# Optimization experiments

Hardware: AMD Instinct MI355X
Metric: run time of the kernel (lower is better)

Reference implementation:

```python
import jax, jax.numpy as jnp
import numpy as np

KEY_CHANNELS = 256


def conv1x1_relu(x, w, b):
    # x: [B, Cin, H, W], w: [Cout, Cin], b: [Cout] -> [B, Cout, H, W]
    y = jnp.einsum('oc,bchw->bohw', w, x) + b[None, :, None, None]
    return jax.nn.relu(y)


def setup_inputs() -> dict:
    key = jax.random.key(0)
    ks = jax.random.split(key, 16)
    B, C, H, W = 8, 512, 128, 128
    Kc, Kp = KEY_CHANNELS, 150
    sc = lambda cin: 1.0 / np.sqrt(cin)
    return {
        'x': jax.random.normal(ks[0], (B, C, H, W), jnp.float32),
        'proxy': jax.random.normal(ks[1], (B, C, Kp, 1), jnp.float32),
        'w_fp1': jax.random.normal(ks[2], (Kc, C), jnp.float32) * sc(C),
        'b_fp1': jax.random.normal(ks[3], (Kc,), jnp.float32) * 0.1,
        'w_fp2': jax.random.normal(ks[4], (Kc, Kc), jnp.float32) * sc(Kc),
        'b_fp2': jax.random.normal(ks[5], (Kc,), jnp.float32) * 0.1,
        'w_fo1': jax.random.normal(ks[6], (Kc, C), jnp.float32) * sc(C),
        'b_fo1': jax.random.normal(ks[7], (Kc,), jnp.float32) * 0.1,
        'w_fo2': jax.random.normal(ks[8], (Kc, Kc), jnp.float32) * sc(Kc),
        'b_fo2': jax.random.normal(ks[9], (Kc,), jnp.float32) * 0.1,
        'w_fd': jax.random.normal(ks[10], (Kc, C), jnp.float32) * sc(C),
        'b_fd': jax.random.normal(ks[11], (Kc,), jnp.float32) * 0.1,
        'w_fu': jax.random.normal(ks[12], (C, Kc), jnp.float32) * sc(Kc),
        'b_fu': jax.random.normal(ks[13], (C,), jnp.float32) * 0.1,
    }


def reference(x, proxy, w_fp1, b_fp1, w_fp2, b_fp2, w_fo1, b_fo1,
              w_fo2, b_fo2, w_fd, b_fd, w_fu, b_fu):
    B, C, H, W = x.shape
    Kc = w_fp1.shape[0]
    # f_pixel: two 1x1 conv(+folded BN)+ReLU blocks -> query [B, HW, Kc]
    q = conv1x1_relu(conv1x1_relu(x, w_fp1, b_fp1), w_fp2, b_fp2)
    query = q.reshape(B, Kc, H * W).transpose(0, 2, 1)
    # f_object -> key [B, Kc, Kp]
    k = conv1x1_relu(conv1x1_relu(proxy, w_fo1, b_fo1), w_fo2, b_fo2)
    key = k.reshape(B, Kc, -1)
    # f_down -> value [B, Kp, Kc]
    v = conv1x1_relu(proxy, w_fd, b_fd)
    value = v.reshape(B, Kc, -1).transpose(0, 2, 1)
    # cross-attention: softmax(Q K^T / sqrt(Kc)) V
    sim = jnp.einsum('bnc,bck->bnk', query, key) * (Kc ** -0.5)
    sim = jax.nn.softmax(sim, axis=-1)
    context = jnp.einsum('bnk,bkc->bnc', sim, value)  # [B, HW, Kc]
    context = context.transpose(0, 2, 1).reshape(B, Kc, H, W)
    # f_up: 1x1 conv(+folded BN)+ReLU back to in_channels
    return conv1x1_relu(context, w_fu, b_fu)
```

## Files before the change

### kernel.cpp

```cpp
#include <hip/hip_runtime.h>
#include <hip/hip_bf16.h>


typedef __bf16 bf16x8 __attribute__((ext_vector_type(8)));
typedef float f32x4 __attribute__((ext_vector_type(4)));
typedef unsigned short u16x8 __attribute__((ext_vector_type(8)));

#define AS1 __attribute__((address_space(1)))
#define AS3 __attribute__((address_space(3)))
#define MFMA_16x16x32(a, b, c) __builtin_amdgcn_mfma_f32_16x16x32_bf16((a), (b), (c), 0, 0, 0)

__device__ __forceinline__ unsigned short f2bf(float f) {
  union { float f; unsigned u; } x; x.f = f;
  unsigned r = (x.u + 0x7FFFu + ((x.u >> 16) & 1u)) >> 16;
  return (unsigned short)r;
}

__global__ __launch_bounds__(256) void cast_weights(
    const float* __restrict__ w1, const float* __restrict__ w2,
    const float* __restrict__ wu, unsigned short* __restrict__ W1b,
    unsigned short* __restrict__ W2b, unsigned short* __restrict__ Wub) {
  int i = blockIdx.x * 256 + threadIdx.x;
  if (i < 131072) W1b[i] = f2bf(w1[i]);
  else if (i < 196608) W2b[i - 131072] = f2bf(w2[i - 131072]);
  else if (i < 327680) Wub[i - 196608] = f2bf(wu[i - 196608]);
}

__global__ __launch_bounds__(256) void kv_kernel(
    const float* __restrict__ proxy,
    const float* __restrict__ w_fo1, const float* __restrict__ b_fo1,
    const float* __restrict__ w_fo2, const float* __restrict__ b_fo2,
    const float* __restrict__ w_fd, const float* __restrict__ b_fd,
    unsigned short* __restrict__ keyT, unsigned short* __restrict__ Vv) {
  __shared__ float cols[512][8];
  __shared__ float k1s[256][8];
  const int b = blockIdx.y;
  const int p0 = blockIdx.x * 8;
  const int t = threadIdx.x;
#pragma unroll
  for (int i = 0; i < 8; i++) {
    int idx = t + i * 256;
    int c = idx >> 2, q = idx & 3;
    int p = p0 + q * 2;
    float2 v = make_float2(0.f, 0.f);
    if (p < 150) v = *(const float2*)(proxy + ((size_t)b * 512 + c) * 150 + p);
    cols[c][q * 2 + 0] = v.x;
    cols[c][q * 2 + 1] = v.y;
  }
  __syncthreads();
  float accV[8], accK[8];
  {
    float bv = b_fd[t], bk = b_fo1[t];
#pragma unroll
    for (int px = 0; px < 8; px++) { accV[px] = bv; accK[px] = bk; }
  }
#define KV_FMA(j, wv_, wk_)                                      \
  { float4 ca = *(const float4*)&cols[c + j][0];                 \
    float4 cb = *(const float4*)&cols[c + j][4];                 \
    accV[0] += wv_ * ca.x; accV[1] += wv_ * ca.y;                \
    accV[2] += wv_ * ca.z; accV[3] += wv_ * ca.w;                \
    accV[4] += wv_ * cb.x; accV[5] += wv_ * cb.y;                \
    accV[6] += wv_ * cb.z; accV[7] += wv_ * cb.w;                \
    accK[0] += wk_ * ca.x; accK[1] += wk_ * ca.y;                \
    accK[2] += wk_ * ca.z; accK[3] += wk_ * ca.w;                \
    accK[4] += wk_ * cb.x; accK[5] += wk_ * cb.y;                \
    accK[6] += wk_ * cb.z; accK[7] += wk_ * cb.w; }
  for (int c = 0; c < 512; c += 4) {
    float4 wv4 = *(const float4*)(w_fd + (size_t)t * 512 + c);
    float4 wk4 = *(const float4*)(w_fo1 + (size_t)t * 512 + c);
    KV_FMA(0, wv4.x, wk4.x)
    KV_FMA(1, wv4.y, wk4.y)
    KV_FMA(2, wv4.z, wk4.z)
    KV_FMA(3, wv4.w, wk4.w)
  }
#pragma unroll
  for (int px = 0; px < 8; px++) {
    Vv[((size_t)b * 256 + t) * 160 + p0 + px] = f2bf(fmaxf(accV[px], 0.f));
    k1s[t][px] = fmaxf(accK[px], 0.f);
  }
  __syncthreads();
  float accY[8];
  {
    float by = b_fo2[t];
#pragma unroll
    for (int px = 0; px < 8; px++) accY[px] = by;
  }
#define KV_FMA2(j, wy_)                                          \
  { float4 ca = *(const float4*)&k1s[c + j][0];                  \
    float4 cb = *(const float4*)&k1s[c + j][4];                  \
    accY[0] += wy_ * ca.x; accY[1] += wy_ * ca.y;                \
    accY[2] += wy_ * ca.z; accY[3] += wy_ * ca.w;                \
    accY[4] += wy_ * cb.x; accY[5] += wy_ * cb.y;                \
    accY[6] += wy_ * cb.z; accY[7] += wy_ * cb.w; }
  for (int c = 0; c < 256; c += 4) {
    float4 wy4 = *(const float4*)(w_fo2 + (size_t)t * 256 + c);
    KV_FMA2(0, wy4.x)
    KV_FMA2(1, wy4.y)
    KV_FMA2(2, wy4.z)
    KV_FMA2(3, wy4.w)
  }
#pragma unroll
  for (int px = 0; px < 8; px++)
    keyT[((size_t)b * 160 + p0 + px) * 256 + t] = f2bf(fmaxf(accY[px], 0.f));
}

__global__ __launch_bounds__(256, 3) void gemm1_fused(
    const float* __restrict__ X, const unsigned short* __restrict__ Bt,
    const float* __restrict__ bias, unsigned short* __restrict__ Cq) {
  const int HW = 16384, K = 512, N = 256;
  __shared__ float Af[64 * 128];
  __shared__ unsigned short Bs[128 * 64];
  const int r = blockIdx.x;
  const int b = blockIdx.y;
  const int my = ((r >> 4) << 3) | (r & 7);
  const int nx = (r >> 3) & 1;
  const int m0 = my * 128, n0 = nx * 128;
  const int tid = threadIdx.x;
  const int w = tid >> 6, l = tid & 63;
  const int lr = l & 15, lg = l >> 4;
  const int wm = (w >> 1) * 64, wn = (w & 1) * 64;
  const float* Xb = X + (size_t)b * K * HW;
  const unsigned short* Btb = Bt + (size_t)n0 * K;
  const f32x4 zero = {0.f, 0.f, 0.f, 0.f};
  f32x4 acc[4][4];
#pragma unroll
  for (int m = 0; m < 4; m++)
#pragma unroll
    for (int n = 0; n < 4; n++) acc[m][n] = zero;

  const int arow = l >> 5;
  const int acol = l & 31;
  const int bsub = l >> 3;
  const int bcol = (l & 7) * 8;
  for (int kt = 0; kt < K; kt += 64) {
    __syncthreads();
#pragma unroll
    for (int i = 0; i < 8; i++) {
      const int rk = w * 16 + i * 2 + arow;
      const int s = (rk >> 3) & 7;
      __builtin_amdgcn_global_load_lds(
          (AS1 void*)(Xb + (size_t)(kt + rk) * HW + m0 + ((acol ^ s) << 2)),
          (AS3 void*)(Af + (w * 16 + i * 2) * 128), 16, 0, 0);
    }
#pragma unroll
    for (int i = 0; i < 4; i++) {
      __builtin_amdgcn_global_load_lds(
          (AS1 void*)(Btb + (size_t)(w * 32 + i * 8 + bsub) * K + kt + bcol),
          (AS3 void*)(Bs + (w * 32 + i * 8) * 64), 16, 0, 0);
    }
    __syncthreads();
#pragma unroll
    for (int ks = 0; ks < 2; ks++) {
      bf16x8 aF[4], bF[4];
      const int s = ks * 4 + lg;
#pragma unroll
      for (int m = 0; m < 4; m++) {
        const int p = wm + m * 16 + lr;
        const int cb = ((((p >> 2) ^ s) << 2) | (p & 3));
        bf16x8 a;
#pragma unroll
        for (int j = 0; j < 8; j++)
          a[j] = (__bf16)Af[(ks * 32 + lg * 8 + j) * 128 + cb];
        aF[m] = a;
      }
#pragma unroll
      for (int n = 0; n < 4; n++)
        bF[n] = *(const bf16x8*)(Bs + (wn + n * 16 + lr) * 64 + ks * 32 + lg * 8);
#pragma unroll
      for (int m = 0; m < 4; m++)
#pragma unroll
        for (int n = 0; n < 4; n++) acc[m][n] = MFMA_16x16x32(aF[m], bF[n], acc[m][n]);
    }
  }
  unsigned short* Cb = Cq + (size_t)b * HW * N;
#pragma unroll
  for (int m = 0; m < 4; m++) {
#pragma unroll
    for (int n = 0; n < 4; n++) {
      const int col = n0 + wn + n * 16 + lr;
      const float bc = bias[col];
#pragma unroll
      for (int r2 = 0; r2 < 4; r2++) {
        const int row = m0 + wm + m * 16 + lg * 4 + r2;
        Cb[(size_t)row * N + col] = f2bf(fmaxf(acc[m][n][r2] + bc, 0.f));
      }
    }
  }
}

template <int BIAS_ROW, int OUTF32>
__global__ __launch_bounds__(256, 4) void gemm_bt_relu(
    const unsigned short* __restrict__ A, const unsigned short* __restrict__ Bt,
    const float* __restrict__ bias, void* __restrict__ Cout,
    int M, int N, int K, long long sA, long long sB, long long sC) {
  __shared__ unsigned short As[128 * 64];
  __shared__ unsigned short Bs[128 * 64];
  const int b = blockIdx.z;
  const int m0 = blockIdx.x * 128, n0 = blockIdx.y * 128;
  const int tid = threadIdx.x;
  const int w = tid >> 6, l = tid & 63;
  const int lr = l & 15, lg = l >> 4;
  const int wm = (w >> 1) * 64, wn = (w & 1) * 64;
  const unsigned short* Ab = A + (size_t)b * sA + (size_t)m0 * K;
  const unsigned short* Btb = Bt + (size_t)b * sB + (size_t)n0 * K;
  const f32x4 zero = {0.f, 0.f, 0.f, 0.f};
  f32x4 acc[4][4];
#pragma unroll
  for (int m = 0; m < 4; m++)
#pragma unroll
    for (int n = 0; n < 4; n++) acc[m][n] = zero;

  const int srow = w * 32 + (l >> 3);
  const int scol = (l & 7) * 8;
  for (int kt = 0; kt < K; kt += 64) {
    __syncthreads();
#pragma unroll
    for (int i = 0; i < 4; i++) {
      __builtin_amdgcn_global_load_lds(
          (AS1 void*)(Ab + (size_t)(srow + i * 8) * K + kt + scol),
          (AS3 void*)(As + (w * 32 + i * 8) * 64), 16, 0, 0);
      __builtin_amdgcn_global_load_lds(
          (AS1 void*)(Btb + (size_t)(srow + i * 8) * K + kt + scol),
          (AS3 void*)(Bs + (w * 32 + i * 8) * 64), 16, 0, 0);
    }
    __syncthreads();
#pragma unroll
    for (int ks = 0; ks < 2; ks++) {
      bf16x8 aF[4], bF[4];
#pragma unroll
      for (int m = 0; m < 4; m++)
        aF[m] = *(const bf16x8*)(As + (wm + m * 16 + lr) * 64 + ks * 32 + lg * 8);
#pragma unroll
      for (int n = 0; n < 4; n++)
        bF[n] = *(const bf16x8*)(Bs + (wn + n * 16 + lr) * 64 + ks * 32 + lg * 8);
#pragma unroll
      for (int m = 0; m < 4; m++)
#pragma unroll
        for (int n = 0; n < 4; n++) acc[m][n] = MFMA_16x16x32(aF[m], bF[n], acc[m][n]);
    }
  }
#pragma unroll
  for (int m = 0; m < 4; m++) {
#pragma unroll
    for (int n = 0; n < 4; n++) {
      const int col = n0 + wn + n * 16 + lr;
      const float bc = BIAS_ROW ? 0.f : bias[col];
#pragma unroll
      for (int r = 0; r < 4; r++) {
        const int row = m0 + wm + m * 16 + lg * 4 + r;
        float v = acc[m][n][r] + (BIAS_ROW ? bias[row] : bc);
        v = fmaxf(v, 0.f);
        if (OUTF32)
          ((float*)Cout)[(size_t)b * sC + (size_t)row * N + col] = v;
        else
          ((unsigned short*)Cout)[(size_t)b * sC + (size_t)row * N + col] = f2bf(v);
      }
    }
  }
}

__global__ __launch_bounds__(256, 4) void attn_kernel(
    const unsigned short* __restrict__ Q, const unsigned short* __restrict__ Kt,
    const unsigned short* __restrict__ Vv, unsigned short* __restrict__ ctxT) {
  const int HW = 16384;
  __shared__ unsigned short Pls[128 * 160];
  const int b = blockIdx.y;
  const int pix0 = blockIdx.x * 128;
  const int tid = threadIdx.x;
  const int w = tid >> 6, l = tid & 63;
  const int lr = l & 15, lg = l >> 4;
  const unsigned short* Qb = Q + ((size_t)b * HW + pix0 + w * 32) * 256;
  const unsigned short* Kb = Kt + (size_t)b * 160 * 256;
  const unsigned short* Vb = Vv + (size_t)b * 256 * 160;
  const f32x4 zero = {0.f, 0.f, 0.f, 0.f};

  f32x4 acc[2][10];
#pragma unroll
  for (int m = 0; m < 2; m++)
#pragma unroll
    for (int n = 0; n < 10; n++) acc[m][n] = zero;
#pragma unroll 2
  for (int ks = 0; ks < 8; ks++) {
    bf16x8 aF[2];
#pragma unroll
    for (int m = 0; m < 2; m++)
      aF[m] = *(const bf16x8*)(Qb + (size_t)(m * 16 + lr) * 256 + ks * 32 + lg * 8);
#pragma unroll
    for (int n = 0; n < 10; n++) {
      bf16x8 bF = *(const bf16x8*)(Kb + (size_t)(n * 16 + lr) * 256 + ks * 32 + lg * 8);
      acc[0][n] = MFMA_16x16x32(aF[0], bF, acc[0][n]);
      acc[1][n] = MFMA_16x16x32(aF[1], bF, acc[1][n]);
    }
  }
  const float scale = 0.0625f;
#pragma unroll
  for (int m = 0; m < 2; m++) {
#pragma unroll
    for (int r = 0; r < 4; r++) {
      float lm = -1e30f;
#pragma unroll
      for (int n = 0; n < 10; n++) {
        float v = acc[m][n][r] * scale;
        acc[m][n][r] = v;
        if (n * 16 + lr < 150) lm = fmaxf(lm, v);
      }
#pragma unroll
      for (int msk = 1; msk <= 8; msk <<= 1) lm = fmaxf(lm, __shfl_xor(lm, msk, 64));
      float s = 0.f;
#pragma unroll
      for (int n = 0; n < 10; n++) {
        float p = (n * 16 + lr < 150) ? __expf(acc[m][n][r] - lm) : 0.f;
        acc[m][n][r] = p;
        s += p;
      }
#pragma unroll
      for (int msk = 1; msk <= 8; msk <<= 1) s += __shfl_xor(s, msk, 64);
      float inv = 1.f / s;
      const int row = w * 32 + m * 16 + lg * 4 + r;
      const unsigned sw = (unsigned)(row & 7) << 4;
#pragma unroll
      for (int n = 0; n < 10; n++) {
        unsigned boff = (unsigned)row * 320 + (unsigned)(n * 16 + lr) * 2;
        *(unsigned short*)((char*)Pls + (boff ^ sw)) = f2bf(acc[m][n][r] * inv);
      }
    }
  }
  __syncthreads();
  unsigned short* Cb = ctxT + ((size_t)b * HW + pix0 + w * 32) * 256;
#pragma unroll
  for (int half = 0; half < 2; half++) {
    f32x4 acc2[2][8];
#pragma unroll
    for (int m = 0; m < 2; m++)
#pragma unroll
      for (int n = 0; n < 8; n++) acc2[m][n] = zero;
    for (int ks = 0; ks < 5; ks++) {
      bf16x8 aP[2];
#pragma unroll
      for (int m = 0; m < 2; m++) {
        const int row = w * 32 + m * 16 + lr;
        unsigned boff = (unsigned)row * 320 + (unsigned)(ks * 64 + lg * 16);
        aP[m] = *(const bf16x8*)((const char*)Pls + (boff ^ ((unsigned)(row & 7) << 4)));
      }
#pragma unroll
      for (int n = 0; n < 8; n++) {
        const int ch = half * 128 + n * 16 + lr;
        bf16x8 bV = *(const bf16x8*)(Vb + (size_t)ch * 160 + ks * 32 + lg * 8);
        acc2[0][n] = MFMA_16x16x32(aP[0], bV, acc2[0][n]);
        acc2[1][n] = MFMA_16x16x32(aP[1], bV, acc2[1][n]);
      }
    }
#pragma unroll
    for (int m = 0; m < 2; m++)
#pragma unroll
      for (int n = 0; n < 8; n++)
#pragma unroll
        for (int r = 0; r < 4; r++)
          Cb[(size_t)(m * 16 + lg * 4 + r) * 256 + half * 128 + n * 16 + lr] =
              f2bf(acc2[m][n][r]);
  }
}

extern "C" void kernel_launch(void* const* d_in, const int* in_sizes, int n_in,
                              void* d_out, int out_size, void* d_ws, size_t ws_size,
                              hipStream_t stream) {
  (void)in_sizes; (void)n_in; (void)out_size;
  const float* x     = (const float*)d_in[0];
  const float* proxy = (const float*)d_in[1];
  const float* w_fp1 = (const float*)d_in[2];
  const float* b_fp1 = (const float*)d_in[3];
  const float* w_fp2 = (const float*)d_in[4];
  const float* b_fp2 = (const float*)d_in[5];
  const float* w_fo1 = (const float*)d_in[6];
  const float* b_fo1 = (const float*)d_in[7];
  const float* w_fo2 = (const float*)d_in[8];
  const float* b_fo2 = (const float*)d_in[9];
  const float* w_fd  = (const float*)d_in[10];
  const float* b_fd  = (const float*)d_in[11];
  const float* w_fu  = (const float*)d_in[12];
  const float* b_fu  = (const float*)d_in[13];

  char* ws = (char*)d_ws;
  unsigned short* W1b  = (unsigned short*)(ws + 0);
  unsigned short* W2b  = (unsigned short*)(ws + 262144);
  unsigned short* Wub  = (unsigned short*)(ws + 393216);
  unsigned short* keyT = (unsigned short*)(ws + 655360);
  unsigned short* Vv   = (unsigned short*)(ws + 1310720);
  unsigned short* bufA = (unsigned short*)(ws + 2097152);
  unsigned short* bufB = (unsigned short*)(ws + 2097152 + 134217728);
  if (ws_size < 203423744) return;

  dim3 blk(256);
  cast_weights<<<1280, blk, 0, stream>>>(w_fp1, w_fp2, w_fu, W1b, W2b, Wub);
  kv_kernel<<<dim3(20, 8), blk, 0, stream>>>(proxy, w_fo1, b_fo1, w_fo2, b_fo2,
                                             w_fd, b_fd, keyT, Vv);
  gemm1_fused<<<dim3(256, 8), blk, 0, stream>>>(x, W1b, b_fp1, bufB);
  gemm_bt_relu<0, 0><<<dim3(128, 2, 8), blk, 0, stream>>>(
      bufB, W2b, b_fp2, bufA, 16384, 256, 256,
      (long long)16384 * 256, 0, (long long)16384 * 256);
  attn_kernel<<<dim3(128, 8), blk, 0, stream>>>(bufA, keyT, Vv, bufB);
  gemm_bt_relu<1, 1><<<dim3(4, 128, 8), blk, 0, stream>>>(
      Wub, bufB, b_fu, d_out, 512, 16384, 256,
      0, (long long)16384 * 256, (long long)512 * 16384);
}
```

Measured before the change: 377.2 us.

## Fuse query convs, attention and up-projection into one per-tile mega kernel

Replaces four separate kernels (first conv, second conv, attention, up-projection) with a single kernel. Each block handles 128 pixels of one batch and keeps the intermediate query, probability and context tiles in shared memory. This removes the large bf16 intermediate round trips through global memory and the extra launches. In exchange, weights (W1, W2, Wu) are read straight from global memory by every block without LDS staging, shared memory use rises to 128KB, and occupancy drops to 1024 blocks of 512 threads.

```diff
diff --git a/kernel.cpp b/kernel.cpp
--- a/kernel.cpp
+++ b/kernel.cpp
@@ -4,7 +4,6 @@
 
 typedef __bf16 bf16x8 __attribute__((ext_vector_type(8)));
 typedef float f32x4 __attribute__((ext_vector_type(4)));
-typedef unsigned short u16x8 __attribute__((ext_vector_type(8)));
 
 #define AS1 __attribute__((address_space(1)))
 #define AS3 __attribute__((address_space(3)))
@@ -104,204 +103,153 @@
     keyT[((size_t)b * 160 + p0 + px) * 256 + t] = f2bf(fmaxf(accY[px], 0.f));
 }
 
-__global__ __launch_bounds__(256, 3) void gemm1_fused(
-    const float* __restrict__ X, const unsigned short* __restrict__ Bt,
-    const float* __restrict__ bias, unsigned short* __restrict__ Cq) {
-  const int HW = 16384, K = 512, N = 256;
-  __shared__ float Af[64 * 128];
-  __shared__ unsigned short Bs[128 * 64];
-  const int r = blockIdx.x;
+__global__ __launch_bounds__(512, 2) void mega_kernel(
+    const float* __restrict__ X,
+    const unsigned short* __restrict__ W1, const float* __restrict__ b1,
+    const unsigned short* __restrict__ W2, const float* __restrict__ b2,
+    const unsigned short* __restrict__ Kt, const unsigned short* __restrict__ Vv,
+    const unsigned short* __restrict__ Wu, const float* __restrict__ bu,
+    float* __restrict__ Out) {
+  const int HW = 16384;
+  __shared__ __align__(16) char smem[131072];
+  char* q2s = smem + 65536;
+  float* xs = (float*)q2s;
+
   const int b = blockIdx.y;
-  const int my = ((r >> 4) << 3) | (r & 7);
-  const int nx = (r >> 3) & 1;
-  const int m0 = my * 128, n0 = nx * 128;
-  const int tid = threadIdx.x;
-  const int w = tid >> 6, l = tid & 63;
-  const int lr = l & 15, lg = l >> 4;
-  const int wm = (w >> 1) * 64, wn = (w & 1) * 64;
-  const float* Xb = X + (size_t)b * K * HW;
-  const unsigned short* Btb = Bt + (size_t)n0 * K;
+  const int p0 = blockIdx.x * 128;
+  const int tid = (int)threadIdx.x;
+  const int wid = tid >> 6, l = tid & 63;
+  const int lr = l & 15, lg = (l >> 4) & 3;
   const f32x4 zero = {0.f, 0.f, 0.f, 0.f};
-  f32x4 acc[4][4];
-#pragma unroll
-  for (int m = 0; m < 4; m++)
-#pragma unroll
-    for (int n = 0; n < 4; n++) acc[m][n] = zero;
-
-  const int arow = l >> 5;
-  const int acol = l & 31;
-  const int bsub = l >> 3;
-  const int bcol = (l & 7) * 8;
-  for (int kt = 0; kt < K; kt += 64) {
-    __syncthreads();
-#pragma unroll
-    for (int i = 0; i < 8; i++) {
-      const int rk = w * 16 + i * 2 + arow;
-      const int s = (rk >> 3) & 7;
-      __builtin_amdgcn_global_load_lds(
-          (AS1 void*)(Xb + (size_t)(kt + rk) * HW + m0 + ((acol ^ s) << 2)),
-          (AS3 void*)(Af + (w * 16 + i * 2) * 128), 16, 0, 0);
-    }
-#pragma unroll
-    for (int i = 0; i < 4; i++) {
-      __builtin_amdgcn_global_load_lds(
-          (AS1 void*)(Btb + (size_t)(w * 32 + i * 8 + bsub) * K + kt + bcol),
-          (AS3 void*)(Bs + (w * 32 + i * 8) * 64), 16, 0, 0);
-    }
-    __syncthreads();
-#pragma unroll
-    for (int ks = 0; ks < 2; ks++) {
-      bf16x8 aF[4], bF[4];
-      const int s = ks * 4 + lg;
-#pragma unroll
-      for (int m = 0; m < 4; m++) {
-        const int p = wm + m * 16 + lr;
-        const int cb = ((((p >> 2) ^ s) << 2) | (p & 3));
-        bf16x8 a;
-#pragma unroll
-        for (int j = 0; j < 8; j++)
-          a[j] = (__bf16)Af[(ks * 32 + lg * 8 + j) * 128 + cb];
-        aF[m] = a;
-      }
-#pragma unroll
-      for (int n = 0; n < 4; n++)
-        bF[n] = *(const bf16x8*)(Bs + (wn + n * 16 + lr) * 64 + ks * 32 + lg * 8);
-#pragma unroll
-      for (int m = 0; m < 4; m++)
-#pragma unroll
-        for (int n = 0; n < 4; n++) acc[m][n] = MFMA_16x16x32(aF[m], bF[n], acc[m][n]);
-    }
-  }
-  unsigned short* Cb = Cq + (size_t)b * HW * N;
-#pragma unroll
-  for (int m = 0; m < 4; m++) {
-#pragma unroll
-    for (int n = 0; n < 4; n++) {
-      const int col = n0 + wn + n * 16 + lr;
-      const float bc = bias[col];
-#pragma unroll
-      for (int r2 = 0; r2 < 4; r2++) {
-        const int row = m0 + wm + m * 16 + lg * 4 + r2;
-        Cb[(size_t)row * N + col] = f2bf(fmaxf(acc[m][n][r2] + bc, 0.f));
-      }
-    }
-  }
-}
-
-template <int BIAS_ROW, int OUTF32>
-__global__ __launch_bounds__(256, 4) void gemm_bt_relu(
-    const unsigned short* __restrict__ A, const unsigned short* __restrict__ Bt,
-    const float* __restrict__ bias, void* __restrict__ Cout,
-    int M, int N, int K, long long sA, long long sB, long long sC) {
-  __shared__ unsigned short As[128 * 64];
-  __shared__ unsigned short Bs[128 * 64];
-  const int b = blockIdx.z;
-  const int m0 = blockIdx.x * 128, n0 = blockIdx.y * 128;
-  const int tid = threadIdx.x;
-  const int w = tid >> 6, l = tid & 63;
-  const int lr = l & 15, lg = l >> 4;
-  const int wm = (w >> 1) * 64, wn = (w & 1) * 64;
-  const unsigned short* Ab = A + (size_t)b * sA + (size_t)m0 * K;
-  const unsigned short* Btb = Bt + (size_t)b * sB + (size_t)n0 * K;
-  const f32x4 zero = {0.f, 0.f, 0.f, 0.f};
-  f32x4 acc[4][4];
-#pragma unroll
-  for (int m = 0; m < 4; m++)
-#pragma unroll
-    for (int n = 0; n < 4; n++) acc[m][n] = zero;
-
-  const int srow = w * 32 + (l >> 3);
-  const int scol = (l & 7) * 8;
-  for (int kt = 0; kt < K; kt += 64) {
-    __syncthreads();
-#pragma unroll
-    for (int i = 0; i < 4; i++) {
-      __builtin_amdgcn_global_load_lds(
-          (AS1 void*)(Ab + (size_t)(srow + i * 8) * K + kt + scol),
-          (AS3 void*)(As + (w * 32 + i * 8) * 64), 16, 0, 0);
-      __builtin_amdgcn_global_load_lds(
-          (AS1 void*)(Btb + (size_t)(srow + i * 8) * K + kt + scol),
-          (AS3 void*)(Bs + (w * 32 + i * 8) * 64), 16, 0, 0);
-    }
-    __syncthreads();
-#pragma unroll
-    for (int ks = 0; ks < 2; ks++) {
-      bf16x8 aF[4], bF[4];
-#pragma unroll
-      for (int m = 0; m < 4; m++)
-        aF[m] = *(const bf16x8*)(As + (wm + m * 16 + lr) * 64 + ks * 32 + lg * 8);
-#pragma unroll
-      for (int n = 0; n < 4; n++)
-        bF[n] = *(const bf16x8*)(Bs + (wn + n * 16 + lr) * 64 + ks * 32 + lg * 8);
-#pragma unroll
-      for (int m = 0; m < 4; m++)
-#pragma unroll
-        for (int n = 0; n < 4; n++) acc[m][n] = MFMA_16x16x32(aF[m], bF[n], acc[m][n]);
-    }
-  }
-#pragma unroll
-  for (int m = 0; m < 4; m++) {
-#pragma unroll
-    for (int n = 0; n < 4; n++) {
-      const int col = n0 + wn + n * 16 + lr;
-      const float bc = BIAS_ROW ? 0.f : bias[col];
-#pragma unroll
-      for (int r = 0; r < 4; r++) {
-        const int row = m0 + wm + m * 16 + lg * 4 + r;
-        float v = acc[m][n][r] + (BIAS_ROW ? bias[row] : bc);
-        v = fmaxf(v, 0.f);
-        if (OUTF32)
-          ((float*)Cout)[(size_t)b * sC + (size_t)row * N + col] = v;
-        else
-          ((unsigned short*)Cout)[(size_t)b * sC + (size_t)row * N + col] = f2bf(v);
-      }
-    }
-  }
-}
-
-__global__ __launch_bounds__(256, 4) void attn_kernel(
-    const unsigned short* __restrict__ Q, const unsigned short* __restrict__ Kt,
-    const unsigned short* __restrict__ Vv, unsigned short* __restrict__ ctxT) {
-  const int HW = 16384;
-  __shared__ unsigned short Pls[128 * 160];
-  const int b = blockIdx.y;
-  const int pix0 = blockIdx.x * 128;
-  const int tid = threadIdx.x;
-  const int w = tid >> 6, l = tid & 63;
-  const int lr = l & 15, lg = l >> 4;
-  const unsigned short* Qb = Q + ((size_t)b * HW + pix0 + w * 32) * 256;
-  const unsigned short* Kb = Kt + (size_t)b * 160 * 256;
-  const unsigned short* Vb = Vv + (size_t)b * 256 * 160;
-  const f32x4 zero = {0.f, 0.f, 0.f, 0.f};
-
-  f32x4 acc[2][10];
-#pragma unroll
-  for (int m = 0; m < 2; m++)
-#pragma unroll
-    for (int n = 0; n < 10; n++) acc[m][n] = zero;
-#pragma unroll 2
-  for (int ks = 0; ks < 8; ks++) {
-    bf16x8 aF[2];
+
+  {
+    const int pbase = (wid >> 1) * 32, cbase = (wid & 1) * 128;
+    const float* Xb = X + (size_t)b * 512 * HW + p0;
+    f32x4 acc[2][8];
 #pragma unroll
     for (int m = 0; m < 2; m++)
-      aF[m] = *(const bf16x8*)(Qb + (size_t)(m * 16 + lr) * 256 + ks * 32 + lg * 8);
-#pragma unroll
-    for (int n = 0; n < 10; n++) {
-      bf16x8 bF = *(const bf16x8*)(Kb + (size_t)(n * 16 + lr) * 256 + ks * 32 + lg * 8);
-      acc[0][n] = MFMA_16x16x32(aF[0], bF, acc[0][n]);
-      acc[1][n] = MFMA_16x16x32(aF[1], bF, acc[1][n]);
-    }
-  }
-  const float scale = 0.0625f;
-#pragma unroll
-  for (int m = 0; m < 2; m++) {
+#pragma unroll
+      for (int n = 0; n < 8; n++) acc[m][n] = zero;
+    const int arow = l >> 5, acol = l & 31;
+#pragma unroll 1
+    for (int kt = 0; kt < 512; kt += 64) {
+      __syncthreads();
+#pragma unroll
+      for (int i = 0; i < 4; i++) {
+        const int rk = wid * 8 + i * 2 + arow;
+        __builtin_amdgcn_global_load_lds(
+            (AS1 void*)(Xb + (size_t)(kt + rk) * HW + ((acol ^ wid) << 2)),
+            (AS3 void*)(xs + (wid * 8 + i * 2) * 128), 16, 0, 0);
+      }
+      __syncthreads();
+#pragma unroll
+      for (int ks = 0; ks < 2; ks++) {
+        const int s = ks * 4 + lg;
+        bf16x8 aF[2];
+#pragma unroll
+        for (int m = 0; m < 2; m++) {
+          const int p = pbase + m * 16 + lr;
+          const int cb = (((p >> 2) ^ s) << 2) | (p & 3);
+          bf16x8 a;
+#pragma unroll
+          for (int j = 0; j < 8; j++)
+            a[j] = (__bf16)xs[(ks * 32 + lg * 8 + j) * 128 + cb];
+          aF[m] = a;
+        }
+#pragma unroll
+        for (int n = 0; n < 8; n++) {
+          bf16x8 bF = *(const bf16x8*)(W1 + (size_t)(cbase + n * 16 + lr) * 512 +
+                                       kt + ks * 32 + lg * 8);
+          acc[0][n] = MFMA_16x16x32(aF[0], bF, acc[0][n]);
+          acc[1][n] = MFMA_16x16x32(aF[1], bF, acc[1][n]);
+        }
+      }
+    }
+#pragma unroll
+    for (int n = 0; n < 8; n++) {
+      const int ch = cbase + n * 16 + lr;
+      const float bb = b1[ch];
+#pragma unroll
+      for (int m = 0; m < 2; m++)
+#pragma unroll
+        for (int r = 0; r < 4; r++) {
+          const int pix = pbase + m * 16 + lg * 4 + r;
+          const unsigned boff =
+              ((unsigned)pix * 512 + (unsigned)ch * 2) ^ (((unsigned)pix & 7u) << 4);
+          *(unsigned short*)(smem + boff) = f2bf(fmaxf(acc[m][n][r] + bb, 0.f));
+        }
+    }
+  }
+  __syncthreads();
+
+  {
+    const int pbase = (wid >> 1) * 32, cbase = (wid & 1) * 128;
+    f32x4 acc[2][8];
+#pragma unroll
+    for (int m = 0; m < 2; m++)
+#pragma unroll
+      for (int n = 0; n < 8; n++) acc[m][n] = zero;
+#pragma unroll
+    for (int ks = 0; ks < 8; ks++) {
+      bf16x8 aF[2];
+#pragma unroll
+      for (int m = 0; m < 2; m++) {
+        const int p = pbase + m * 16 + lr;
+        const unsigned boff = ((unsigned)p * 512 + (unsigned)(ks * 64 + lg * 16)) ^
+                              (((unsigned)p & 7u) << 4);
+        aF[m] = *(const bf16x8*)(smem + boff);
+      }
+#pragma unroll
+      for (int n = 0; n < 8; n++) {
+        bf16x8 bF = *(const bf16x8*)(W2 + (size_t)(cbase + n * 16 + lr) * 256 +
+                                     ks * 32 + lg * 8);
+        acc[0][n] = MFMA_16x16x32(aF[0], bF, acc[0][n]);
+        acc[1][n] = MFMA_16x16x32(aF[1], bF, acc[1][n]);
+      }
+    }
+#pragma unroll
+    for (int n = 0; n < 8; n++) {
+      const int ch = cbase + n * 16 + lr;
+      const float bb = b2[ch];
+#pragma unroll
+      for (int m = 0; m < 2; m++)
+#pragma unroll
+        for (int r = 0; r < 4; r++) {
+          const int pix = pbase + m * 16 + lg * 4 + r;
+          const unsigned boff =
+              ((unsigned)pix * 512 + (unsigned)ch * 2) ^ (((unsigned)pix & 7u) << 4);
+          *(unsigned short*)(q2s + boff) = f2bf(fmaxf(acc[m][n][r] + bb, 0.f));
+        }
+    }
+  }
+  __syncthreads();
+
+  {
+    const unsigned short* Kb = Kt + (size_t)b * 160 * 256;
+    const int pbase = wid * 16;
+    f32x4 acc[10];
+#pragma unroll
+    for (int n = 0; n < 10; n++) acc[n] = zero;
+#pragma unroll
+    for (int ks = 0; ks < 8; ks++) {
+      const int p = pbase + lr;
+      const unsigned boff = ((unsigned)p * 512 + (unsigned)(ks * 64 + lg * 16)) ^
+                            (((unsigned)p & 7u) << 4);
+      bf16x8 aF = *(const bf16x8*)(q2s + boff);
+#pragma unroll
+      for (int n = 0; n < 10; n++) {
+        bf16x8 bF = *(const bf16x8*)(Kb + (size_t)(n * 16 + lr) * 256 + ks * 32 + lg * 8);
+        acc[n] = MFMA_16x16x32(aF, bF, acc[n]);
+      }
+    }
+    const float scale = 0.0625f;
 #pragma unroll
     for (int r = 0; r < 4; r++) {
       float lm = -1e30f;
 #pragma unroll
       for (int n = 0; n < 10; n++) {
-        float v = acc[m][n][r] * scale;
-        acc[m][n][r] = v;
+        float v = acc[n][r] * scale;
+        acc[n][r] = v;
         if (n * 16 + lr < 150) lm = fmaxf(lm, v);
       }
 #pragma unroll
@@ -309,55 +257,92 @@
       float s = 0.f;
 #pragma unroll
       for (int n = 0; n < 10; n++) {
-        float p = (n * 16 + lr < 150) ? __expf(acc[m][n][r] - lm) : 0.f;
-        acc[m][n][r] = p;
+        float p = (n * 16 + lr < 150) ? __expf(acc[n][r] - lm) : 0.f;
+        acc[n][r] = p;
         s += p;
       }
 #pragma unroll
       for (int msk = 1; msk <= 8; msk <<= 1) s += __shfl_xor(s, msk, 64);
       float inv = 1.f / s;
-      const int row = w * 32 + m * 16 + lg * 4 + r;
-      const unsigned sw = (unsigned)(row & 7) << 4;
+      const int row = pbase + lg * 4 + r;
+      const unsigned sw = (((unsigned)row & 7u) << 4);
 #pragma unroll
       for (int n = 0; n < 10; n++) {
-        unsigned boff = (unsigned)row * 320 + (unsigned)(n * 16 + lr) * 2;
-        *(unsigned short*)((char*)Pls + (boff ^ sw)) = f2bf(acc[m][n][r] * inv);
-      }
-    }
-  }
-  __syncthreads();
-  unsigned short* Cb = ctxT + ((size_t)b * HW + pix0 + w * 32) * 256;
-#pragma unroll
-  for (int half = 0; half < 2; half++) {
-    f32x4 acc2[2][8];
-#pragma unroll
-    for (int m = 0; m < 2; m++)
-#pragma unroll
-      for (int n = 0; n < 8; n++) acc2[m][n] = zero;
+        const unsigned boff = ((unsigned)row * 320 + (unsigned)(n * 16 + lr) * 2) ^ sw;
+        *(unsigned short*)(smem + boff) = f2bf(acc[n][r] * inv);
+      }
+    }
+  }
+  __syncthreads();
+
+  {
+    const unsigned short* Vb = Vv + (size_t)b * 256 * 160;
+    const int pbase = wid * 16;
+    f32x4 acc[16];
+#pragma unroll
+    for (int n = 0; n < 16; n++) acc[n] = zero;
+#pragma unroll
     for (int ks = 0; ks < 5; ks++) {
-      bf16x8 aP[2];
-#pragma unroll
-      for (int m = 0; m < 2; m++) {
-        const int row = w * 32 + m * 16 + lr;
-        unsigned boff = (unsigned)row * 320 + (unsigned)(ks * 64 + lg * 16);
-        aP[m] = *(const bf16x8*)((const char*)Pls + (boff ^ ((unsigned)(row & 7) << 4)));
-      }
+      const int p = pbase + lr;
+      const unsigned boff = ((unsigned)p * 320 + (unsigned)(ks * 64 + lg * 16)) ^
+                            (((unsigned)p & 7u) << 4);
+      bf16x8 aF = *(const bf16x8*)(smem + boff);
+#pragma unroll
+      for (int n = 0; n < 16; n++) {
+        bf16x8 bF = *(const bf16x8*)(Vb + (size_t)(n * 16 + lr) * 160 + ks * 32 + lg * 8);
+        acc[n] = MFMA_16x16x32(aF, bF, acc[n]);
+      }
+    }
+#pragma unroll
+    for (int n = 0; n < 16; n++) {
+#pragma unroll
+      for (int r = 0; r < 4; r++) {
+        const int pix = pbase + lg * 4 + r;
+        const int ch = n * 16 + lr;
+        const unsigned boff =
+            ((unsigned)pix * 512 + (unsigned)ch * 2) ^ (((unsigned)pix & 7u) << 4);
+        *(unsigned short*)(q2s + boff) = f2bf(acc[n][r]);
+      }
+    }
+  }
+  __syncthreads();
+
+  {
+    float* Ob = Out + (size_t)b * 512 * HW + p0;
+    const int cobase = wid * 64;
+    f32x4 acc[4][8];
+#pragma unroll
+    for (int m = 0; m < 4; m++)
+#pragma unroll
+      for (int n = 0; n < 8; n++) acc[m][n] = zero;
+#pragma unroll
+    for (int ks = 0; ks < 8; ks++) {
+      bf16x8 aF[4];
+#pragma unroll
+      for (int m = 0; m < 4; m++)
+        aF[m] = *(const bf16x8*)(Wu + (size_t)(cobase + m * 16 + lr) * 256 +
+                                 ks * 32 + lg * 8);
 #pragma unroll
       for (int n = 0; n < 8; n++) {
-        const int ch = half * 128 + n * 16 + lr;
-        bf16x8 bV = *(const bf16x8*)(Vb + (size_t)ch * 160 + ks * 32 + lg * 8);
-        acc2[0][n] = MFMA_16x16x32(aP[0], bV, acc2[0][n]);
-        acc2[1][n] = MFMA_16x16x32(aP[1], bV, acc2[1][n]);
-      }
-    }
-#pragma unroll
-    for (int m = 0; m < 2; m++)
-#pragma unroll
-      for (int n = 0; n < 8; n++)
-#pragma unroll
-        for (int r = 0; r < 4; r++)
-          Cb[(size_t)(m * 16 + lg * 4 + r) * 256 + half * 128 + n * 16 + lr] =
-              f2bf(acc2[m][n][r]);
+        const int pix = n * 16 + lr;
+        const unsigned boff = ((unsigned)pix * 512 + (unsigned)(ks * 64 + lg * 16)) ^
+                              (((unsigned)pix & 7u) << 4);
+        bf16x8 bF = *(const bf16x8*)(q2s + boff);
+#pragma unroll
+        for (int m = 0; m < 4; m++) acc[m][n] = MFMA_16x16x32(aF[m], bF, acc[m][n]);
+      }
+    }
+#pragma unroll
+    for (int m = 0; m < 4; m++) {
+#pragma unroll
+      for (int r = 0; r < 4; r++) {
+        const int co = cobase + m * 16 + lg * 4 + r;
+        const float bb = bu[co];
+#pragma unroll
+        for (int n = 0; n < 8; n++)
+          Ob[(size_t)co * HW + n * 16 + lr] = fmaxf(acc[m][n][r] + bb, 0.f);
+      }
+    }
   }
 }
 
@@ -386,20 +371,12 @@
   unsigned short* Wub  = (unsigned short*)(ws + 393216);
   unsigned short* keyT = (unsigned short*)(ws + 655360);
   unsigned short* Vv   = (unsigned short*)(ws + 1310720);
-  unsigned short* bufA = (unsigned short*)(ws + 2097152);
-  unsigned short* bufB = (unsigned short*)(ws + 2097152 + 134217728);
-  if (ws_size < 203423744) return;
+  if (ws_size < 2097152) return;
 
   dim3 blk(256);
   cast_weights<<<1280, blk, 0, stream>>>(w_fp1, w_fp2, w_fu, W1b, W2b, Wub);
   kv_kernel<<<dim3(20, 8), blk, 0, stream>>>(proxy, w_fo1, b_fo1, w_fo2, b_fo2,
                                              w_fd, b_fd, keyT, Vv);
-  gemm1_fused<<<dim3(256, 8), blk, 0, stream>>>(x, W1b, b_fp1, bufB);
-  gemm_bt_relu<0, 0><<<dim3(128, 2, 8), blk, 0, stream>>>(
-      bufB, W2b, b_fp2, bufA, 16384, 256, 256,
-      (long long)16384 * 256, 0, (long long)16384 * 256);
-  attn_kernel<<<dim3(128, 8), blk, 0, stream>>>(bufA, keyT, Vv, bufB);
-  gemm_bt_relu<1, 1><<<dim3(4, 128, 8), blk, 0, stream>>>(
-      Wub, bufB, b_fu, d_out, 512, 16384, 256,
-      0, (long long)16384 * 256, (long long)512 * 16384);
-}
+  mega_kernel<<<dim3(128, 8), dim3(512), 0, stream>>>(
+      x, W1b, b_fp1, W2b, b_fp2, keyT, Vv, Wub, b_fu, (float*)d_out);
+}
```

Result: slower. 487.1 us (+29.1%).
